# Kernel optimization log

Hardware: AMD Instinct MI355X
Metric: run time of the kernel (lower is better)

The kernel has to match this reference:

```python
import jax, jax.numpy as jnp
import numpy as np

B, T, C = 2, 2048, 2048
NH, NKV, HD = 16, 8, 256
SOFTCAP = 50.0
ROPE_BASE = 10000.0


def setup_inputs() -> dict:
    key = jax.random.key(0)
    ks = jax.random.split(key, 5)
    s = 0.02
    return {
        "X": jax.random.normal(ks[0], (B, T, C), dtype=jnp.float32),
        "Wq": jax.random.normal(ks[1], (C, NH * HD), dtype=jnp.float32) * s,
        "Wk": jax.random.normal(ks[2], (C, NKV * HD), dtype=jnp.float32) * s,
        "Wv": jax.random.normal(ks[3], (C, NKV * HD), dtype=jnp.float32) * s,
        "Wo": jax.random.normal(ks[4], (NH * HD, C), dtype=jnp.float32) * s,
    }


def _rotate_half(x):
    x1, x2 = x[..., : x.shape[-1] // 2], x[..., x.shape[-1] // 2 :]
    return jnp.concatenate((-x2, x1), axis=-1)


def _rope_cos_sin(t, head_dim, dtype):
    inv_freq = 1.0 / ROPE_BASE ** (
        jnp.arange(0, head_dim, 2, dtype=jnp.int32).astype(jnp.float32) / head_dim
    )  # [HD/2]
    pos = jnp.arange(t, dtype=jnp.float32)  # [T]
    freqs = pos[:, None] * inv_freq[None, :]  # [T, HD/2]
    emb = jnp.concatenate((freqs, freqs), axis=-1)  # [T, HD]
    # shape [1, 1, T, HD] to broadcast over (B, H, T, HD)
    return (
        jnp.cos(emb).astype(dtype)[None, None],
        jnp.sin(emb).astype(dtype)[None, None],
    )


def reference(X, Wq, Wk, Wv, Wo):
    b, t, c = X.shape
    n_rep = NH // NKV

    q = (X @ Wq).reshape(b, t, NH, HD).transpose(0, 2, 1, 3)   # [B,NH,T,HD]
    k = (X @ Wk).reshape(b, t, NKV, HD).transpose(0, 2, 1, 3)  # [B,NKV,T,HD]
    v = (X @ Wv).reshape(b, t, NKV, HD).transpose(0, 2, 1, 3)

    cos, sin = _rope_cos_sin(t, HD, X.dtype)
    q = q * cos + _rotate_half(q) * sin
    k = k * cos + _rotate_half(k) * sin

    # repeat_kv (GQA): [B,NKV,T,HD] -> [B,NH,T,HD]
    k = jnp.repeat(k, n_rep, axis=1)
    v = jnp.repeat(v, n_rep, axis=1)

    scale = 256.0 ** (-0.5)  # hardcoded in source
    att = jnp.einsum("bhqd,bhkd->bhqk", q, k) * scale
    # tanh logit softcapping
    att = SOFTCAP * jnp.tanh(att / SOFTCAP)
    # causal mask
    causal = jnp.tril(jnp.ones((t, t), dtype=bool))
    att = jnp.where(causal[None, None], att, -jnp.inf)
    att = jax.nn.softmax(att, axis=-1)

    y = jnp.einsum("bhqk,bhkd->bhqd", att, v)  # [B,NH,T,HD]
    y = y.transpose(0, 2, 1, 3).reshape(b, t, NH * HD)
    return y @ Wo
```

## Files before the change

kernel.cpp:

```cpp
#include <hip/hip_runtime.h>
#include <hip/hip_bf16.h>

#define NHD 16
#define NKVH 8
#define HDIM 256
#define TSEQ 2048
#define BATCH 2

typedef unsigned int   u32;
typedef unsigned short u16;

typedef __attribute__((ext_vector_type(8))) short bf16x8;
typedef __attribute__((ext_vector_type(4))) float floatx4;

__device__ inline u32 cvt2bf(float lo, float hi) {
  u32 r;
  asm("v_cvt_pk_bf16_f32 %0, %1, %2" : "=v"(r) : "v"(lo), "v"(hi));
  return r;
}
__device__ inline u16 f2bf(float f) {
  union { float f; u32 i; } v; v.f = f;
  u32 r = v.i + 0x7fffu + ((v.i >> 16) & 1u);
  return (u16)(r >> 16);
}
__device__ inline float bf2f(u16 u) {
  union { u32 i; float f; } v; v.i = ((u32)u) << 16; return v.f;
}
__device__ inline float fexp2(float x) {
  float r; asm("v_exp_f32 %0, %1" : "=v"(r) : "v"(x)); return r;
}
__device__ inline float frcp(float x) {
  float r; asm("v_rcp_f32 %0, %1" : "=v"(r) : "v"(x)); return r;
}

typedef const __attribute__((address_space(1))) u32* gptr_t;
typedef __attribute__((address_space(3))) u32* lptr_t;
__device__ inline void gl_lds16(const void* g, void* l) {
  __builtin_amdgcn_global_load_lds((gptr_t)g, (lptr_t)l, 16, 0, 0);
}

__global__ __launch_bounds__(256) void tconv_k(
    const float* __restrict__ in, u16* __restrict__ out, int R, int Cc)
{
  __shared__ float tile[64][65];
  const int r0 = blockIdx.y * 64, c0 = blockIdx.x * 64;
  const int tr = threadIdx.x >> 4;
  const int tc = (threadIdx.x & 15) * 4;
#pragma unroll
  for (int j = 0; j < 4; ++j) {
    float4 v = *(const float4*)(in + (size_t)(r0 + tr + j * 16) * Cc + c0 + tc);
    tile[tr + j * 16][tc + 0] = v.x;
    tile[tr + j * 16][tc + 1] = v.y;
    tile[tr + j * 16][tc + 2] = v.z;
    tile[tr + j * 16][tc + 3] = v.w;
  }
  __syncthreads();
#pragma unroll
  for (int j = 0; j < 4; ++j) {
    int c = tr + j * 16;
    u16 o[4];
#pragma unroll
    for (int i = 0; i < 4; ++i) o[i] = f2bf(tile[tc + i][c]);
    *(uint2*)(out + (size_t)(c0 + c) * R + r0 + tc) = *(const uint2*)o;
  }
}

__global__ __launch_bounds__(256) void xconv_k(
    const float* __restrict__ in, u16* __restrict__ out)
{
  size_t i = (size_t)blockIdx.x * 256 + threadIdx.x;
  float4 a = *(const float4*)(in + i * 8);
  float4 b = *(const float4*)(in + i * 8 + 4);
  uint4 o;
  o.x = cvt2bf(a.x, a.y); o.y = cvt2bf(a.z, a.w);
  o.z = cvt2bf(b.x, b.y); o.w = cvt2bf(b.z, b.w);
  *(uint4*)(out + i * 8) = o;
}

template<int EPI, int BM>
__global__ __launch_bounds__(512, 2) void gemm256_k(
    const u16* __restrict__ Ab, const u16* __restrict__ BTp,
    void* __restrict__ Op, int M, int N, int K)
{
  constexpr int NI = BM / 32;
  constexpr int AI = BM / 64;
  __shared__ u16 LA[2][BM * 64];
  __shared__ u16 LB[2][256 * 64];
  const int t = threadIdx.x;
  const int lane = t & 63, wave = t >> 6;
  const int lg = lane >> 4, l15 = lane & 15;
  const int wm = wave >> 2, wn = wave & 3;
  const int mtiles = M / BM;
  const int mt = (int)blockIdx.x % mtiles, nt = (int)blockIdx.x / mtiles;
  const int m0 = mt * BM, n0 = nt << 8;

  const int arow = wave * (BM / 8) + (lane >> 3);
  const int ska  = ((lane & 7) ^ (arow & 7)) << 3;
  const int brow = wave * 32 + (lane >> 3);
  const int skb  = ((lane & 7) ^ (brow & 7)) << 3;
  const u16* Ag = Ab  + (size_t)(m0 + arow) * K + ska;
  const u16* Bg = BTp + (size_t)(n0 + brow) * K + skb;

  auto STAGE = [&](int k0, int sel) {
#pragma unroll
    for (int q = 0; q < AI; ++q)
      gl_lds16(Ag + k0 + (size_t)q * 8 * K, &LA[sel][(wave * (BM / 8) + q * 8) * 64]);
#pragma unroll
    for (int q = 0; q < 4; ++q)
      gl_lds16(Bg + k0 + (size_t)q * 8 * K, &LB[sel][(wave * 32 + q * 8) * 64]);
  };

  floatx4 acc[NI][4];
#pragma unroll
  for (int i = 0; i < NI; ++i)
#pragma unroll
    for (int j = 0; j < 4; ++j) acc[i][j] = (floatx4){0.f, 0.f, 0.f, 0.f};

  STAGE(0, 0);
  const int KT = K >> 6;
  for (int kt = 0; kt < KT; ++kt) {
    const int sel = kt & 1;
    if (kt + 1 < KT) {
      STAGE((kt + 1) << 6, sel ^ 1);
      if constexpr (BM == 256) asm volatile("s_waitcnt vmcnt(8)" ::: "memory");
      else                     asm volatile("s_waitcnt vmcnt(6)" ::: "memory");
    } else {
      asm volatile("s_waitcnt vmcnt(0)" ::: "memory");
    }
    __builtin_amdgcn_s_barrier();
    __builtin_amdgcn_sched_barrier(0);
    __builtin_amdgcn_s_setprio(1);
#pragma unroll
    for (int ks = 0; ks < 2; ++ks) {
      const int c = (ks << 2) + lg;
      bf16x8 bfv[4];
#pragma unroll
      for (int j = 0; j < 4; ++j) {
        int row = wn * 64 + (j << 4) + l15;
        bfv[j] = *(const bf16x8*)(&LB[sel][row * 64 + ((c ^ (row & 7)) << 3)]);
      }
#pragma unroll
      for (int i = 0; i < NI; ++i) {
        int row = wm * (BM / 2) + (i << 4) + l15;
        bf16x8 af = *(const bf16x8*)(&LA[sel][row * 64 + ((c ^ (row & 7)) << 3)]);
#pragma unroll
        for (int j = 0; j < 4; ++j)
          acc[i][j] = __builtin_amdgcn_mfma_f32_16x16x32_bf16(af, bfv[j], acc[i][j], 0, 0, 0);
      }
    }
    __builtin_amdgcn_s_setprio(0);
    __builtin_amdgcn_s_barrier();
  }

#pragma unroll
  for (int i = 0; i < NI; ++i) {
#pragma unroll
    for (int j = 0; j < 4; ++j) {
#pragma unroll
      for (int r = 0; r < 4; ++r) {
        int m = m0 + wm * (BM / 2) + (i << 4) + (lg << 2) + r;
        int n = n0 + wn * 64 + (j << 4) + l15;
        float v = acc[i][j][r];
        int bb = m >> 11, tt = m & 2047;
        if (EPI == 0) {
          ((float*)Op)[(size_t)m * N + n] = v;
        } else if (EPI == 1) {
          int h = n >> 8, d = n & 255;
          ((u16*)Op)[(((size_t)bb * NHD + h) * TSEQ + tt) * HDIM + d] = f2bf(v);
        } else {
          if (n < 2048) {
            int h = n >> 8, d = n & 255;
            ((u16*)Op)[(((size_t)bb * NKVH + h) * TSEQ + tt) * HDIM + d] = f2bf(v);
          } else {
            int n2 = n - 2048;
            int h = n2 >> 8, d = n2 & 255;
            ((u16*)Op)[8388608u + (((size_t)bb * NKVH + h) * HDIM + d) * TSEQ + tt] = f2bf(v);
          }
        }
      }
    }
  }
}

__global__ __launch_bounds__(256) void rope_k(u16* buf) {
  size_t idx = (size_t)blockIdx.x * 256 + threadIdx.x;
  int d = (int)(idx & 127);
  size_t rest = idx >> 7;
  int tt = (int)(rest & (TSEQ - 1));
  float invf = exp2f(-(float)d * 0.103810253f);
  float th = (float)tt * invf;
  float sn, cs;
  sincosf(th, &sn, &cs);
  size_t base = rest * HDIM;
  float x1 = bf2f(buf[base + d]);
  float x2 = bf2f(buf[base + d + 128]);
  buf[base + d]       = f2bf(x1 * cs - x2 * sn);
  buf[base + d + 128] = f2bf(x2 * cs + x1 * sn);
}

__global__ __launch_bounds__(256, 2) void attn_k(
    const u16* __restrict__ Q, const u16* __restrict__ Kb,
    const u16* __restrict__ Vt, u16* __restrict__ Y)
{
  __shared__ u16 Ks2[2][32 * 256];
  __shared__ u16 Vs2[2][256 * 32];
  __shared__ u16 Ps[4 * 16 * 32];
  __shared__ float Ls[4][16];
  const int t = threadIdx.x, lane = t & 63, w = t >> 6;
  const int lg = lane >> 4, l15 = lane & 15;
  const int qt = 31 - (int)blockIdx.y;
  const int h = (int)blockIdx.x >> 1, b = (int)blockIdx.x & 1;
  const int hkv = h >> 1;

  const u16* Kg = Kb + ((size_t)(b * NKVH + hkv)) * TSEQ * HDIM;
  const u16* Vg = Vt + ((size_t)(b * NKVH + hkv)) * HDIM * TSEQ;

  int koff[4], voff[4];
#pragma unroll
  for (int q = 0; q < 4; ++q) {
    int krow = w * 8 + q * 2 + (lane >> 5);
    int kcc  = lane & 31;
    koff[q] = krow * 256 + ((kcc ^ (krow & 7)) << 3);
    int vd  = w * 64 + q * 16 + (lane >> 2);
    voff[q] = vd * TSEQ + (((lane & 3) ^ ((vd >> 2) & 3)) << 3);
  }

  auto STAGE = [&](int st, int sel) {
    const u16* kbase = Kg + (size_t)st * (32 * 256);
    const u16* vbase = Vg + st * 32;
#pragma unroll
    for (int q = 0; q < 4; ++q)
      gl_lds16(kbase + koff[q], &Ks2[sel][(w * 8 + q * 2) * 256]);
#pragma unroll
    for (int q = 0; q < 4; ++q)
      gl_lds16(vbase + voff[q], &Vs2[sel][(w * 64 + q * 16) * 32]);
  };

  const u16* Qg = Q + (((size_t)(b * NHD + h)) * TSEQ + qt * 64 + w * 16 + l15) * HDIM;
  bf16x8 qf[8];
#pragma unroll
  for (int ks = 0; ks < 8; ++ks) qf[ks] = *(const bf16x8*)(Qg + ks * 32 + lg * 8);

  floatx4 accY[16];
#pragma unroll
  for (int i = 0; i < 16; ++i) accY[i] = (floatx4){0.f, 0.f, 0.f, 0.f};
  float rsum = 0.f;

  const int qglob = qt * 64 + w * 16 + l15;
  const int qmaxw = qt * 64 + w * 16 + 15;
  const int nst = 2 * qt + 2;
  const int fps = (l15 ^ (l15 >> 2)) & 3;

  STAGE(0, 0);
  for (int st = 0; st < nst; ++st) {
    const int sel = st & 1;
    if (st + 1 < nst) {
      STAGE(st + 1, sel ^ 1);
      asm volatile("s_waitcnt vmcnt(8)" ::: "memory");
    } else {
      asm volatile("s_waitcnt vmcnt(0)" ::: "memory");
    }
    __builtin_amdgcn_s_barrier();
    __builtin_amdgcn_sched_barrier(0);

    if (st * 32 <= qmaxw) {
      __builtin_amdgcn_s_setprio(1);
#pragma unroll
      for (int stile = 0; stile < 2; ++stile) {
        floatx4 sa = (floatx4){0.f, 0.f, 0.f, 0.f};
#pragma unroll
        for (int ks = 0; ks < 8; ++ks) {
          int row = (stile << 4) + l15;
          int c = (ks << 2) + lg;
          bf16x8 kf = *(const bf16x8*)((const char*)Ks2[sel] +
                        row * 512 + ((c ^ (row & 7)) << 4));
          sa = __builtin_amdgcn_mfma_f32_16x16x32_bf16(kf, qf[ks], sa, 0, 0, 0);
        }
        int sbase = st * 32 + (stile << 4) + (lg << 2);
        float p[4];
#pragma unroll
        for (int r = 0; r < 4; ++r) {
          float u = fexp2(sa[r] * 0.0036067376f);
          float pv = fexp2(-144.26950408f * frcp(u + 1.0f));
          pv = (sbase + r <= qglob) ? pv : 0.0f;
          p[r] = pv;
          rsum += pv;
        }
        uint2 pw;
        pw.x = cvt2bf(p[0], p[1]);
        pw.y = cvt2bf(p[2], p[3]);
        int o = (stile << 5) + (lg << 3);
        int gran = (o >> 4) ^ fps;
        *(uint2*)((char*)Ps + (w << 10) + l15 * 64 + (gran << 4) + (o & 15)) = pw;
      }
      {
        bf16x8 pf = *(const bf16x8*)((const char*)Ps + (w << 10) + l15 * 64 +
                      ((lg ^ fps) << 4));
#pragma unroll
        for (int dt = 0; dt < 16; ++dt) {
          int row = (dt << 4) + l15;
          bf16x8 vf = *(const bf16x8*)((const char*)Vs2[sel] +
                        row * 64 + ((lg ^ ((row >> 2) & 3)) << 4));
          accY[dt] = __builtin_amdgcn_mfma_f32_16x16x32_bf16(pf, vf, accY[dt], 0, 0, 0);
        }
      }
      __builtin_amdgcn_s_setprio(0);
    }
    __builtin_amdgcn_s_barrier();
  }

  rsum += __shfl_xor(rsum, 16);
  rsum += __shfl_xor(rsum, 32);
  if (lane < 16) Ls[w][l15] = rsum;
  __syncthreads();
  float inv[4];
#pragma unroll
  for (int r = 0; r < 4; ++r) inv[r] = 1.0f / Ls[w][(lg << 2) + r];

  u16* Yg = Y + ((size_t)(b * TSEQ + qt * 64 + w * 16)) * (NHD * HDIM) + h * HDIM;
#pragma unroll
  for (int dt = 0; dt < 16; ++dt)
#pragma unroll
    for (int r = 0; r < 4; ++r)
      Yg[(size_t)((lg << 2) + r) * (NHD * HDIM) + (dt << 4) + l15] =
          f2bf(accY[dt][r] * inv[r]);
}

extern "C" void kernel_launch(void* const* d_in, const int* in_sizes, int n_in,
                              void* d_out, int out_size, void* d_ws, size_t ws_size,
                              hipStream_t stream) {
  const float* X  = (const float*)d_in[0];
  const float* Wq = (const float*)d_in[1];
  const float* Wk = (const float*)d_in[2];
  const float* Wv = (const float*)d_in[3];
  const float* Wo = (const float*)d_in[4];
  float* out = (float*)d_out;

  u16* ws   = (u16*)d_ws;
  u16* XB   = ws;
  u16* WT   = ws + 8388608;
  u16* Qb   = ws + 16777216;
  u16* KVb  = ws + 33554432;
  u16* Yb   = ws;
  u16* WoT  = ws + 16777216;

  dim3 blk(256);
  xconv_k<<<dim3(4096), blk, 0, stream>>>(X, XB);
  tconv_k<<<dim3(64, 32), blk, 0, stream>>>(Wq, WT, 2048, 4096);
  gemm256_k<1, 256><<<dim3(16 * 16), dim3(512), 0, stream>>>(XB, WT, Qb, 4096, 4096, 2048);
  tconv_k<<<dim3(32, 32), blk, 0, stream>>>(Wk, WT, 2048, 2048);
  tconv_k<<<dim3(32, 32), blk, 0, stream>>>(Wv, WT + (size_t)2048 * 2048, 2048, 2048);
  gemm256_k<3, 256><<<dim3(16 * 16), dim3(512), 0, stream>>>(XB, WT, KVb, 4096, 4096, 2048);
  rope_k<<<dim3((BATCH * NHD  * TSEQ * 128) / 256), blk, 0, stream>>>(Qb);
  rope_k<<<dim3((BATCH * NKVH * TSEQ * 128) / 256), blk, 0, stream>>>(KVb);
  attn_k<<<dim3(32, 32), blk, 0, stream>>>(Qb, KVb, KVb + 8388608, Yb);
  tconv_k<<<dim3(32, 64), blk, 0, stream>>>(Wo, WoT, 4096, 2048);
  gemm256_k<0, 128><<<dim3(32 * 8), dim3(512), 0, stream>>>(Yb, WoT, out, 4096, 2048, 4096);
}
```

Before: 424.9 us.

## Add phased-pipelined 256x256 GEMM for QKV projections and merge RoPE launches

```diff
diff --git a/kernel.cpp b/kernel.cpp
--- a/kernel.cpp
+++ b/kernel.cpp
@@ -75,6 +75,130 @@
   o.x = cvt2bf(a.x, a.y); o.y = cvt2bf(a.z, a.w);
   o.z = cvt2bf(b.x, b.y); o.w = cvt2bf(b.z, b.w);
   *(uint4*)(out + i * 8) = o;
+}
+
+template<int EPI>
+__global__ __launch_bounds__(512, 2) void gemmq_k(
+    const u16* __restrict__ Ab, const u16* __restrict__ BTp,
+    void* __restrict__ Op, int M, int N, int K)
+{
+  constexpr int BUF = 256 * 64;
+  __shared__ u16 LA[2 * BUF];
+  __shared__ u16 LB[2 * BUF];
+  const int t = threadIdx.x;
+  const int lane = t & 63, wave = t >> 6;
+  const int lg = lane >> 4, l15 = lane & 15;
+  const int wm = wave >> 2, wn = wave & 3;
+  const int mtiles = M >> 8;
+  const int mt = (int)blockIdx.x % mtiles, nt = (int)blockIdx.x / mtiles;
+  const int m0 = mt << 8, n0 = nt << 8;
+
+  auto STAGE_A = [&](int kt, int h) {
+    const int slot = kt & 1, k0 = kt << 6;
+#pragma unroll
+    for (int q = 0; q < 2; ++q) {
+      int idx = wave * 2 + q;
+      int kh = idx >> 3, g = (idx >> 1) & 3, rc = idx & 1;
+      int row = h * 128 + rc * 64;
+      gl_lds16(Ab + (size_t)(m0 + row + lane) * K + k0 + kh * 32 + g * 8,
+               &LA[slot * BUF + (((kh << 2) + g) * 256 + row) * 8]);
+    }
+  };
+  auto STAGE_B = [&](int kt, int h) {
+    const int slot = kt & 1, k0 = kt << 6;
+#pragma unroll
+    for (int q = 0; q < 2; ++q) {
+      int idx = wave * 2 + q;
+      int kh = idx >> 3, g = (idx >> 1) & 3, rc = idx & 1;
+      int row = h * 128 + rc * 64;
+      gl_lds16(BTp + (size_t)(n0 + row + lane) * K + k0 + kh * 32 + g * 8,
+               &LB[slot * BUF + (((kh << 2) + g) * 256 + row) * 8]);
+    }
+  };
+
+  floatx4 acc[8][4];
+#pragma unroll
+  for (int i = 0; i < 8; ++i)
+#pragma unroll
+    for (int j = 0; j < 4; ++j) acc[i][j] = (floatx4){0.f, 0.f, 0.f, 0.f};
+
+  STAGE_A(0, 0); STAGE_A(0, 1);
+  STAGE_B(0, 0); STAGE_B(0, 1);
+  STAGE_B(1, 0); STAGE_B(1, 1);
+
+  const int KT = K >> 6;
+  for (int kt = 0; kt < KT; ++kt) {
+    const int slot = kt & 1;
+    bf16x8 bfv[2][4];
+#pragma unroll
+    for (int p = 0; p < 4; ++p) {
+      if (p == 0) {
+        if (kt + 1 < KT) asm volatile("s_waitcnt vmcnt(4)" ::: "memory");
+        else             asm volatile("s_waitcnt vmcnt(0)" ::: "memory");
+      }
+      __builtin_amdgcn_s_barrier();
+      if (p == 0) {
+#pragma unroll
+        for (int kh = 0; kh < 2; ++kh)
+#pragma unroll
+          for (int j = 0; j < 4; ++j)
+            bfv[kh][j] = *(const bf16x8*)(
+                &LB[slot * BUF + (((kh << 2) + lg) * 256 + wn * 64 + (j << 4) + l15) * 8]);
+      }
+      bf16x8 af[2][2];
+#pragma unroll
+      for (int fl = 0; fl < 2; ++fl)
+#pragma unroll
+        for (int kh = 0; kh < 2; ++kh)
+          af[fl][kh] = *(const bf16x8*)(
+              &LA[slot * BUF + (((kh << 2) + lg) * 256 + wm * 128 + ((2 * p + fl) << 4) + l15) * 8]);
+
+      if (p == 0 && kt + 1 < KT) STAGE_A(kt + 1, 0);
+      if (p == 1 && kt + 1 < KT) STAGE_A(kt + 1, 1);
+      if (p == 2 && kt + 2 < KT) STAGE_B(kt + 2, 0);
+      if (p == 3 && kt + 2 < KT) STAGE_B(kt + 2, 1);
+
+      asm volatile("s_waitcnt lgkmcnt(0)" ::: "memory");
+      __builtin_amdgcn_sched_barrier(0);
+      __builtin_amdgcn_s_setprio(1);
+#pragma unroll
+      for (int fl = 0; fl < 2; ++fl)
+#pragma unroll
+        for (int j = 0; j < 4; ++j)
+#pragma unroll
+          for (int kh = 0; kh < 2; ++kh)
+            acc[2 * p + fl][j] = __builtin_amdgcn_mfma_f32_16x16x32_bf16(
+                af[fl][kh], bfv[kh][j], acc[2 * p + fl][j], 0, 0, 0);
+      __builtin_amdgcn_s_setprio(0);
+    }
+  }
+
+#pragma unroll
+  for (int i = 0; i < 8; ++i) {
+#pragma unroll
+    for (int j = 0; j < 4; ++j) {
+#pragma unroll
+      for (int r = 0; r < 4; ++r) {
+        int m = m0 + wm * 128 + (i << 4) + (lg << 2) + r;
+        int n = n0 + wn * 64 + (j << 4) + l15;
+        float v = acc[i][j][r];
+        int bb = m >> 11, tt = m & 2047;
+        if (EPI == 1) {
+          int h = n >> 8, d = n & 255;
+          ((u16*)Op)[(((size_t)bb * NHD + h) * TSEQ + tt) * HDIM + d] = f2bf(v);
+        } else {
+          if (n < 2048) {
+            int h = n >> 8, d = n & 255;
+            ((u16*)Op)[(((size_t)bb * NKVH + h) * TSEQ + tt) * HDIM + d] = f2bf(v);
+          } else {
+            int n2 = n - 2048;
+            int h = n2 >> 8, d = n2 & 255;
+            ((u16*)Op)[8388608u + (((size_t)bb * NKVH + h) * HDIM + d) * TSEQ + tt] = f2bf(v);
+          }
+        }
+      }
+    }
+  }
 }
 
 template<int EPI, int BM>
@@ -160,30 +284,18 @@
       for (int r = 0; r < 4; ++r) {
         int m = m0 + wm * (BM / 2) + (i << 4) + (lg << 2) + r;
         int n = n0 + wn * 64 + (j << 4) + l15;
-        float v = acc[i][j][r];
-        int bb = m >> 11, tt = m & 2047;
-        if (EPI == 0) {
-          ((float*)Op)[(size_t)m * N + n] = v;
-        } else if (EPI == 1) {
-          int h = n >> 8, d = n & 255;
-          ((u16*)Op)[(((size_t)bb * NHD + h) * TSEQ + tt) * HDIM + d] = f2bf(v);
-        } else {
-          if (n < 2048) {
-            int h = n >> 8, d = n & 255;
-            ((u16*)Op)[(((size_t)bb * NKVH + h) * TSEQ + tt) * HDIM + d] = f2bf(v);
-          } else {
-            int n2 = n - 2048;
-            int h = n2 >> 8, d = n2 & 255;
-            ((u16*)Op)[8388608u + (((size_t)bb * NKVH + h) * HDIM + d) * TSEQ + tt] = f2bf(v);
-          }
-        }
-      }
-    }
-  }
-}
-
-__global__ __launch_bounds__(256) void rope_k(u16* buf) {
+        ((float*)Op)[(size_t)m * N + n] = acc[i][j][r];
+      }
+    }
+  }
+}
+
+__global__ __launch_bounds__(256) void rope_k(u16* Qb, u16* Kb) {
   size_t idx = (size_t)blockIdx.x * 256 + threadIdx.x;
+  const size_t qtot = (size_t)BATCH * NHD * TSEQ * 128;
+  u16* buf;
+  if (idx < qtot) buf = Qb;
+  else { idx -= qtot; buf = Kb; }
   int d = (int)(idx & 127);
   size_t rest = idx >> 7;
   int tt = (int)(rest & (TSEQ - 1));
@@ -347,12 +459,11 @@
   dim3 blk(256);
   xconv_k<<<dim3(4096), blk, 0, stream>>>(X, XB);
   tconv_k<<<dim3(64, 32), blk, 0, stream>>>(Wq, WT, 2048, 4096);
-  gemm256_k<1, 256><<<dim3(16 * 16), dim3(512), 0, stream>>>(XB, WT, Qb, 4096, 4096, 2048);
+  gemmq_k<1><<<dim3(16 * 16), dim3(512), 0, stream>>>(XB, WT, Qb, 4096, 4096, 2048);
   tconv_k<<<dim3(32, 32), blk, 0, stream>>>(Wk, WT, 2048, 2048);
   tconv_k<<<dim3(32, 32), blk, 0, stream>>>(Wv, WT + (size_t)2048 * 2048, 2048, 2048);
-  gemm256_k<3, 256><<<dim3(16 * 16), dim3(512), 0, stream>>>(XB, WT, KVb, 4096, 4096, 2048);
-  rope_k<<<dim3((BATCH * NHD  * TSEQ * 128) / 256), blk, 0, stream>>>(Qb);
-  rope_k<<<dim3((BATCH * NKVH * TSEQ * 128) / 256), blk, 0, stream>>>(KVb);
+  gemmq_k<3><<<dim3(16 * 16), dim3(512), 0, stream>>>(XB, WT, KVb, 4096, 4096, 2048);
+  rope_k<<<dim3((BATCH * (NHD + NKVH) * TSEQ * 128) / 256), blk, 0, stream>>>(Qb, KVb);
   attn_k<<<dim3(32, 32), blk, 0, stream>>>(Qb, KVb, KVb + 8388608, Yb);
   tconv_k<<<dim3(32, 64), blk, 0, stream>>>(Wo, WoT, 4096, 2048);
   gemm256_k<0, 128><<<dim3(32 * 8), dim3(512), 0, stream>>>(Yb, WoT, out, 4096, 2048, 4096);
```

Result: slower. 444.3 us (+4.6%).

## Single-buffer V in LDS via register staging to fit three attention blocks per CU

Applied to the files above, without the earlier changes.

```diff
diff --git a/kernel.cpp b/kernel.cpp
--- a/kernel.cpp
+++ b/kernel.cpp
@@ -182,8 +182,12 @@
   }
 }
 
-__global__ __launch_bounds__(256) void rope_k(u16* buf) {
+__global__ __launch_bounds__(256) void rope_k(u16* Qb, u16* Kb) {
   size_t idx = (size_t)blockIdx.x * 256 + threadIdx.x;
+  const size_t qtot = (size_t)BATCH * NHD * TSEQ * 128;
+  u16* buf;
+  if (idx < qtot) buf = Qb;
+  else { idx -= qtot; buf = Kb; }
   int d = (int)(idx & 127);
   size_t rest = idx >> 7;
   int tt = (int)(rest & (TSEQ - 1));
@@ -198,12 +202,12 @@
   buf[base + d + 128] = f2bf(x2 * cs + x1 * sn);
 }
 
-__global__ __launch_bounds__(256, 2) void attn_k(
+__global__ __launch_bounds__(256, 3) void attn_k(
     const u16* __restrict__ Q, const u16* __restrict__ Kb,
     const u16* __restrict__ Vt, u16* __restrict__ Y)
 {
   __shared__ u16 Ks2[2][32 * 256];
-  __shared__ u16 Vs2[2][256 * 32];
+  __shared__ u16 Vs[256 * 32];
   __shared__ u16 Ps[4 * 16 * 32];
   __shared__ float Ls[4][16];
   const int t = threadIdx.x, lane = t & 63, w = t >> 6;
@@ -216,6 +220,7 @@
   const u16* Vg = Vt + ((size_t)(b * NKVH + hkv)) * HDIM * TSEQ;
 
   int koff[4], voff[4];
+  int vdst[4];
 #pragma unroll
   for (int q = 0; q < 4; ++q) {
     int krow = w * 8 + q * 2 + (lane >> 5);
@@ -223,17 +228,21 @@
     koff[q] = krow * 256 + ((kcc ^ (krow & 7)) << 3);
     int vd  = w * 64 + q * 16 + (lane >> 2);
     voff[q] = vd * TSEQ + (((lane & 3) ^ ((vd >> 2) & 3)) << 3);
-  }
-
-  auto STAGE = [&](int st, int sel) {
+    vdst[q] = (w * 64 + q * 16) * 32 + lane * 8;
+  }
+
+  auto STAGE_K = [&](int st, int sel) {
     const u16* kbase = Kg + (size_t)st * (32 * 256);
-    const u16* vbase = Vg + st * 32;
 #pragma unroll
     for (int q = 0; q < 4; ++q)
       gl_lds16(kbase + koff[q], &Ks2[sel][(w * 8 + q * 2) * 256]);
+  };
+  uint4 vv[4];
+  auto LOAD_V = [&](int st) {
+    const u16* vbase = Vg + st * 32;
 #pragma unroll
     for (int q = 0; q < 4; ++q)
-      gl_lds16(vbase + voff[q], &Vs2[sel][(w * 64 + q * 16) * 32]);
+      vv[q] = *(const uint4*)(vbase + voff[q]);
   };
 
   const u16* Qg = Q + (((size_t)(b * NHD + h)) * TSEQ + qt * 64 + w * 16 + l15) * HDIM;
@@ -251,15 +260,21 @@
   const int nst = 2 * qt + 2;
   const int fps = (l15 ^ (l15 >> 2)) & 3;
 
-  STAGE(0, 0);
+  STAGE_K(0, 0);
+  LOAD_V(0);
   for (int st = 0; st < nst; ++st) {
     const int sel = st & 1;
+    asm volatile("s_waitcnt vmcnt(0)" ::: "memory");
+    __builtin_amdgcn_s_barrier();
+#pragma unroll
+    for (int q = 0; q < 4; ++q)
+      *(uint4*)(&Vs[vdst[q]]) = vv[q];
     if (st + 1 < nst) {
-      STAGE(st + 1, sel ^ 1);
-      asm volatile("s_waitcnt vmcnt(8)" ::: "memory");
-    } else {
-      asm volatile("s_waitcnt vmcnt(0)" ::: "memory");
-    }
+      STAGE_K(st + 1, sel ^ 1);
+      LOAD_V(st + 1);
+    }
+    asm volatile("s_waitcnt lgkmcnt(0)" ::: "memory");
+    __builtin_amdgcn_sched_barrier(0);
     __builtin_amdgcn_s_barrier();
     __builtin_amdgcn_sched_barrier(0);
 
@@ -299,7 +314,7 @@
 #pragma unroll
         for (int dt = 0; dt < 16; ++dt) {
           int row = (dt << 4) + l15;
-          bf16x8 vf = *(const bf16x8*)((const char*)Vs2[sel] +
+          bf16x8 vf = *(const bf16x8*)((const char*)Vs +
                         row * 64 + ((lg ^ ((row >> 2) & 3)) << 4));
           accY[dt] = __builtin_amdgcn_mfma_f32_16x16x32_bf16(pf, vf, accY[dt], 0, 0, 0);
         }
@@ -351,8 +366,7 @@
   tconv_k<<<dim3(32, 32), blk, 0, stream>>>(Wk, WT, 2048, 2048);
   tconv_k<<<dim3(32, 32), blk, 0, stream>>>(Wv, WT + (size_t)2048 * 2048, 2048, 2048);
   gemm256_k<3, 256><<<dim3(16 * 16), dim3(512), 0, stream>>>(XB, WT, KVb, 4096, 4096, 2048);
-  rope_k<<<dim3((BATCH * NHD  * TSEQ * 128) / 256), blk, 0, stream>>>(Qb);
-  rope_k<<<dim3((BATCH * NKVH * TSEQ * 128) / 256), blk, 0, stream>>>(KVb);
+  rope_k<<<dim3((BATCH * (NHD + NKVH) * TSEQ * 128) / 256), blk, 0, stream>>>(Qb, KVb);
   attn_k<<<dim3(32, 32), blk, 0, stream>>>(Qb, KVb, KVb + 8388608, Yb);
   tconv_k<<<dim3(32, 64), blk, 0, stream>>>(Wo, WoT, 4096, 2048);
   gemm256_k<0, 128><<<dim3(32 * 8), dim3(512), 0, stream>>>(Yb, WoT, out, 4096, 2048, 4096);
```

Result: slower. 511.8 us (+20.4%).

## Merge prep conversions and rope launches, split QK accumulator chain

Applied to the files above, without the earlier changes.

```diff
diff --git a/kernel.cpp b/kernel.cpp
--- a/kernel.cpp
+++ b/kernel.cpp
@@ -39,13 +39,13 @@
   __builtin_amdgcn_global_load_lds((gptr_t)g, (lptr_t)l, 16, 0, 0);
 }
 
-__global__ __launch_bounds__(256) void tconv_k(
-    const float* __restrict__ in, u16* __restrict__ out, int R, int Cc)
-{
+__device__ inline void tconv_body(const float* __restrict__ in,
+                                  u16* __restrict__ out, int R, int Cc,
+                                  int bx, int by, int tid) {
   __shared__ float tile[64][65];
-  const int r0 = blockIdx.y * 64, c0 = blockIdx.x * 64;
-  const int tr = threadIdx.x >> 4;
-  const int tc = (threadIdx.x & 15) * 4;
+  const int r0 = by * 64, c0 = bx * 64;
+  const int tr = tid >> 4;
+  const int tc = (tid & 15) * 4;
 #pragma unroll
   for (int j = 0; j < 4; ++j) {
     float4 v = *(const float4*)(in + (size_t)(r0 + tr + j * 16) * Cc + c0 + tc);
@@ -63,6 +63,12 @@
     for (int i = 0; i < 4; ++i) o[i] = f2bf(tile[tc + i][c]);
     *(uint2*)(out + (size_t)(c0 + c) * R + r0 + tc) = *(const uint2*)o;
   }
+}
+
+__global__ __launch_bounds__(256) void tconv_k(
+    const float* __restrict__ in, u16* __restrict__ out, int R, int Cc)
+{
+  tconv_body(in, out, R, Cc, blockIdx.x, blockIdx.y, threadIdx.x);
 }
 
 __global__ __launch_bounds__(256) void xconv_k(
@@ -75,6 +81,32 @@
   o.x = cvt2bf(a.x, a.y); o.y = cvt2bf(a.z, a.w);
   o.z = cvt2bf(b.x, b.y); o.w = cvt2bf(b.z, b.w);
   *(uint4*)(out + i * 8) = o;
+}
+
+__global__ __launch_bounds__(256) void prep_k(
+    const float* __restrict__ X,  const float* __restrict__ Wq,
+    const float* __restrict__ Wk, const float* __restrict__ Wv,
+    u16* __restrict__ XB, u16* __restrict__ WqT, u16* __restrict__ WkvT)
+{
+  const int bid = blockIdx.x, tid = threadIdx.x;
+  if (bid < 4096) {
+    size_t i = (size_t)bid * 256 + tid;
+    float4 a = *(const float4*)(X + i * 8);
+    float4 b = *(const float4*)(X + i * 8 + 4);
+    uint4 o;
+    o.x = cvt2bf(a.x, a.y); o.y = cvt2bf(a.z, a.w);
+    o.z = cvt2bf(b.x, b.y); o.w = cvt2bf(b.z, b.w);
+    *(uint4*)(XB + i * 8) = o;
+  } else if (bid < 6144) {
+    int idx = bid - 4096;
+    tconv_body(Wq, WqT, 2048, 4096, idx & 63, idx >> 6, tid);
+  } else if (bid < 7168) {
+    int idx = bid - 6144;
+    tconv_body(Wk, WkvT, 2048, 2048, idx & 31, idx >> 5, tid);
+  } else {
+    int idx = bid - 7168;
+    tconv_body(Wv, WkvT + (size_t)2048 * 2048, 2048, 2048, idx & 31, idx >> 5, tid);
+  }
 }
 
 template<int EPI, int BM>
@@ -182,8 +214,12 @@
   }
 }
 
-__global__ __launch_bounds__(256) void rope_k(u16* buf) {
+__global__ __launch_bounds__(256) void rope_k(u16* Qb, u16* Kb) {
   size_t idx = (size_t)blockIdx.x * 256 + threadIdx.x;
+  const size_t qtot = (size_t)BATCH * NHD * TSEQ * 128;
+  u16* buf;
+  if (idx < qtot) buf = Qb;
+  else { idx -= qtot; buf = Kb; }
   int d = (int)(idx & 127);
   size_t rest = idx >> 7;
   int tt = (int)(rest & (TSEQ - 1));
@@ -267,20 +303,24 @@
       __builtin_amdgcn_s_setprio(1);
 #pragma unroll
       for (int stile = 0; stile < 2; ++stile) {
-        floatx4 sa = (floatx4){0.f, 0.f, 0.f, 0.f};
+        floatx4 sa0 = (floatx4){0.f, 0.f, 0.f, 0.f};
+        floatx4 sa1 = (floatx4){0.f, 0.f, 0.f, 0.f};
 #pragma unroll
         for (int ks = 0; ks < 8; ++ks) {
           int row = (stile << 4) + l15;
           int c = (ks << 2) + lg;
           bf16x8 kf = *(const bf16x8*)((const char*)Ks2[sel] +
                         row * 512 + ((c ^ (row & 7)) << 4));
-          sa = __builtin_amdgcn_mfma_f32_16x16x32_bf16(kf, qf[ks], sa, 0, 0, 0);
+          if (ks & 1)
+            sa1 = __builtin_amdgcn_mfma_f32_16x16x32_bf16(kf, qf[ks], sa1, 0, 0, 0);
+          else
+            sa0 = __builtin_amdgcn_mfma_f32_16x16x32_bf16(kf, qf[ks], sa0, 0, 0, 0);
         }
         int sbase = st * 32 + (stile << 4) + (lg << 2);
         float p[4];
 #pragma unroll
         for (int r = 0; r < 4; ++r) {
-          float u = fexp2(sa[r] * 0.0036067376f);
+          float u = fexp2((sa0[r] + sa1[r]) * 0.0036067376f);
           float pv = fexp2(-144.26950408f * frcp(u + 1.0f));
           pv = (sbase + r <= qglob) ? pv : 0.0f;
           p[r] = pv;
@@ -336,24 +376,42 @@
   const float* Wo = (const float*)d_in[4];
   float* out = (float*)d_out;
 
-  u16* ws   = (u16*)d_ws;
-  u16* XB   = ws;
-  u16* WT   = ws + 8388608;
-  u16* Qb   = ws + 16777216;
-  u16* KVb  = ws + 33554432;
-  u16* Yb   = ws;
-  u16* WoT  = ws + 16777216;
-
+  u16* ws = (u16*)d_ws;
   dim3 blk(256);
-  xconv_k<<<dim3(4096), blk, 0, stream>>>(X, XB);
-  tconv_k<<<dim3(64, 32), blk, 0, stream>>>(Wq, WT, 2048, 4096);
-  gemm256_k<1, 256><<<dim3(16 * 16), dim3(512), 0, stream>>>(XB, WT, Qb, 4096, 4096, 2048);
-  tconv_k<<<dim3(32, 32), blk, 0, stream>>>(Wk, WT, 2048, 2048);
-  tconv_k<<<dim3(32, 32), blk, 0, stream>>>(Wv, WT + (size_t)2048 * 2048, 2048, 2048);
-  gemm256_k<3, 256><<<dim3(16 * 16), dim3(512), 0, stream>>>(XB, WT, KVb, 4096, 4096, 2048);
-  rope_k<<<dim3((BATCH * NHD  * TSEQ * 128) / 256), blk, 0, stream>>>(Qb);
-  rope_k<<<dim3((BATCH * NKVH * TSEQ * 128) / 256), blk, 0, stream>>>(KVb);
-  attn_k<<<dim3(32, 32), blk, 0, stream>>>(Qb, KVb, KVb + 8388608, Yb);
-  tconv_k<<<dim3(32, 64), blk, 0, stream>>>(Wo, WoT, 4096, 2048);
-  gemm256_k<0, 128><<<dim3(32 * 8), dim3(512), 0, stream>>>(Yb, WoT, out, 4096, 2048, 4096);
-}
+
+  if (ws_size >= (size_t)117440512) {
+    u16* XB   = ws;
+    u16* WqT  = ws + 8388608;
+    u16* WkvT = ws + 16777216;
+    u16* Qb   = ws + 25165824;
+    u16* KVb  = ws + 41943040;
+    u16* Yb   = ws;
+    u16* WoT  = ws + 25165824;
+
+    prep_k<<<dim3(8192), blk, 0, stream>>>(X, Wq, Wk, Wv, XB, WqT, WkvT);
+    gemm256_k<1, 256><<<dim3(256), dim3(512), 0, stream>>>(XB, WqT,  Qb,  4096, 4096, 2048);
+    gemm256_k<3, 256><<<dim3(256), dim3(512), 0, stream>>>(XB, WkvT, KVb, 4096, 4096, 2048);
+    rope_k<<<dim3(49152), blk, 0, stream>>>(Qb, KVb);
+    attn_k<<<dim3(32, 32), blk, 0, stream>>>(Qb, KVb, KVb + 8388608, Yb);
+    tconv_k<<<dim3(32, 64), blk, 0, stream>>>(Wo, WoT, 4096, 2048);
+    gemm256_k<0, 128><<<dim3(256), dim3(512), 0, stream>>>(Yb, WoT, out, 4096, 2048, 4096);
+  } else {
+    u16* XB   = ws;
+    u16* WT   = ws + 8388608;
+    u16* Qb   = ws + 16777216;
+    u16* KVb  = ws + 33554432;
+    u16* Yb   = ws;
+    u16* WoT  = ws + 16777216;
+
+    xconv_k<<<dim3(4096), blk, 0, stream>>>(X, XB);
+    tconv_k<<<dim3(64, 32), blk, 0, stream>>>(Wq, WT, 2048, 4096);
+    gemm256_k<1, 256><<<dim3(256), dim3(512), 0, stream>>>(XB, WT, Qb, 4096, 4096, 2048);
+    tconv_k<<<dim3(32, 32), blk, 0, stream>>>(Wk, WT, 2048, 2048);
+    tconv_k<<<dim3(32, 32), blk, 0, stream>>>(Wv, WT + (size_t)2048 * 2048, 2048, 2048);
+    gemm256_k<3, 256><<<dim3(256), dim3(512), 0, stream>>>(XB, WT, KVb, 4096, 4096, 2048);
+    rope_k<<<dim3(49152), blk, 0, stream>>>(Qb, KVb);
+    attn_k<<<dim3(32, 32), blk, 0, stream>>>(Qb, KVb, KVb + 8388608, Yb);
+    tconv_k<<<dim3(32, 64), blk, 0, stream>>>(Wo, WoT, 4096, 2048);
+    gemm256_k<0, 128><<<dim3(256), dim3(512), 0, stream>>>(Yb, WoT, out, 4096, 2048, 4096);
+  }
+}
```

After: 421.6 us. Within noise of the previous version (-0.8%).
